# Performance work log

Measured on AMD Instinct MI355X. Metric: run time of the kernel, lower is better.

## Reference

```python
import jax, jax.numpy as jnp
import numpy as np

B, S, D, H, HD = 1, 2048, 3072, 24, 128
FFN = int(D / 3 * 8)  # 8192
ADALN = 256
NORM_EPS = 1e-6
QK_EPS = 1e-5
AXES_DIMS = (16, 56, 56)
AXES_LENS = (64, 128, 128)
THETA = 256.0


def rmsnorm(x, w, eps):
    var = jnp.mean(jnp.square(x), axis=-1, keepdims=True)
    return x * jax.lax.rsqrt(var + eps) * w


def apply_rope(x, cos, sin):
    # x: [B,S,H,HD]; cos/sin: [B,S,HD//2] (broadcast over heads, matching freqs_cis.unsqueeze(2))
    xr = x[..., 0::2]
    xi = x[..., 1::2]
    c = cos[:, :, None, :]
    s = sin[:, :, None, :]
    or_ = xr * c - xi * s
    oi_ = xr * s + xi * c
    return jnp.stack([or_, oi_], axis=-1).reshape(x.shape)


def rope_angles(ids):
    # ids: [B,S,3] int; returns angles [B,S,HD//2] concatenated per axis like RopeEmbedder
    parts = []
    for d, idx_axis in zip(AXES_DIMS, range(len(AXES_DIMS))):
        freqs = 1.0 / (THETA ** (jnp.arange(0, d, 2, dtype=jnp.float32) / d))  # [d/2]
        ang = ids[..., idx_axis].astype(jnp.float32)[..., None] * freqs  # [B,S,d/2]
        parts.append(ang)
    return jnp.concatenate(parts, axis=-1)  # [B,S,64]


def setup_inputs() -> dict:
    key = jax.random.key(0)
    ks = jax.random.split(key, 20)
    w = 0.02
    ids = jnp.concatenate([
        jax.random.randint(ks[15], (B, S, 1), 0, AXES_LENS[0]),
        jax.random.randint(ks[16], (B, S, 1), 0, AXES_LENS[1]),
        jax.random.randint(ks[17], (B, S, 1), 0, AXES_LENS[2]),
    ], axis=-1)
    return {
        "x": jax.random.normal(ks[0], (B, S, D), jnp.float32),
        "adaln_input": jax.random.normal(ks[1], (B, ADALN), jnp.float32),
        "attn_mask": jnp.ones((B, S), dtype=bool),
        "ids": ids,
        "attn_norm1_w": jnp.ones((D,), jnp.float32),
        "attn_norm2_w": jnp.ones((D,), jnp.float32),
        "ffn_norm1_w": jnp.ones((D,), jnp.float32),
        "ffn_norm2_w": jnp.ones((D,), jnp.float32),
        "norm_q_w": jnp.ones((HD,), jnp.float32),
        "norm_k_w": jnp.ones((HD,), jnp.float32),
        "wq": jax.random.normal(ks[2], (D, D), jnp.float32) * w,
        "wk": jax.random.normal(ks[3], (D, D), jnp.float32) * w,
        "wv": jax.random.normal(ks[4], (D, D), jnp.float32) * w,
        "wo": jax.random.normal(ks[5], (D, D), jnp.float32) * w,
        "w1": jax.random.normal(ks[6], (D, FFN), jnp.float32) * w,
        "w2": jax.random.normal(ks[7], (FFN, D), jnp.float32) * w,
        "w3": jax.random.normal(ks[8], (D, FFN), jnp.float32) * w,
        "adaln_w": jax.random.normal(ks[9], (ADALN, 4 * D), jnp.float32) * w,
        "adaln_b": jnp.zeros((4 * D,), jnp.float32),
    }


def block_forward(x, adaln_input, attn_mask, ids,
                  attn_norm1_w, attn_norm2_w, ffn_norm1_w, ffn_norm2_w,
                  norm_q_w, norm_k_w, wq, wk, wv, wo, w1, w2, w3,
                  adaln_w, adaln_b):
    ang = rope_angles(ids)
    cos, sin = jnp.cos(ang), jnp.sin(ang)

    mod = adaln_input @ adaln_w + adaln_b
    scale_msa, gate_msa, scale_mlp, gate_mlp = jnp.split(mod[:, None, :], 4, axis=2)
    gate_msa, gate_mlp = jnp.tanh(gate_msa), jnp.tanh(gate_mlp)
    scale_msa, scale_mlp = 1.0 + scale_msa, 1.0 + scale_mlp

    # Attention branch
    xs = rmsnorm(x, attn_norm1_w, NORM_EPS) * scale_msa  # [B,S,D]
    q = (xs @ wq).reshape(B, S, H, HD)
    k = (xs @ wk).reshape(B, S, H, HD)
    v = (xs @ wv).reshape(B, S, H, HD)
    q = rmsnorm(q, norm_q_w, QK_EPS)
    k = rmsnorm(k, norm_k_w, QK_EPS)
    q = apply_rope(q, cos, sin)
    k = apply_rope(k, cos, sin)

    scores = jnp.einsum('bqhd,bkhd->bhqk', q, k) / jnp.sqrt(jnp.float32(HD))
    neg = jnp.finfo(scores.dtype).min
    scores = jnp.where(attn_mask[:, None, None, :], scores, neg)
    probs = jax.nn.softmax(scores, axis=-1)
    attn = jnp.einsum('bhqk,bkhd->bqhd', probs, v).reshape(B, S, D)
    attn_out = attn @ wo

    x = x + gate_msa * rmsnorm(attn_out, attn_norm2_w, NORM_EPS)

    # FFN branch (SwiGLU)
    xf = rmsnorm(x, ffn_norm1_w, NORM_EPS) * scale_mlp
    h = jax.nn.silu(xf @ w1) * (xf @ w3)
    ffn_out = h @ w2
    x = x + gate_mlp * rmsnorm(ffn_out, ffn_norm2_w, NORM_EPS)
    return x


def reference(x, adaln_input, attn_mask, ids,
              attn_norm1_w, attn_norm2_w, ffn_norm1_w, ffn_norm2_w,
              norm_q_w, norm_k_w, wq, wk, wv, wo, w1, w2, w3,
              adaln_w, adaln_b):
    return block_forward(x, adaln_input, attn_mask, ids,
                         attn_norm1_w, attn_norm2_w, ffn_norm1_w, ffn_norm2_w,
                         norm_q_w, norm_k_w, wq, wk, wv, wo, w1, w2, w3,
                         adaln_w, adaln_b)
```

## Files before the change

### kernel.cpp

```cpp
#include <hip/hip_runtime.h>

#define AS1 __attribute__((address_space(1)))
#define AS3 __attribute__((address_space(3)))

typedef __bf16 bf16;
using bf16x8 = __attribute__((ext_vector_type(8))) __bf16;
using bf16x4 = __attribute__((ext_vector_type(4))) __bf16;
using bf16x2 = __attribute__((ext_vector_type(2))) __bf16;
using f32x4  = __attribute__((ext_vector_type(4))) float;


__device__ inline float wsum(float v) {
#pragma unroll
  for (int o = 32; o; o >>= 1) v += __shfl_xor(v, o, 64);
  return v;
}

template <int EPI>
__global__ __launch_bounds__(512, 1) void gemm256(
    const bf16* __restrict__ A, const bf16* __restrict__ Bt, void* __restrict__ Cv,
    int K, int lda, int ldb, int ldc, long long kOff, long long sC) {
  __shared__ bf16 lds[2][2][256 * 64];
  const int t = threadIdx.x;
  const int lane = t & 63, wid = t >> 6;
  const int wm = wid >> 2, wn = wid & 3;
  const int row16 = lane & 15, kg = lane >> 4;
  const int m0 = blockIdx.x * 256, n0 = blockIdx.y * 256;
  const int NT = K >> 6;
  const int sgran = (lane & 7) ^ (lane >> 3);
  A += (long long)blockIdx.z * kOff;
  Bt += (long long)blockIdx.z * kOff;

  auto stageA = [&](int buf, int r, int tk) {
    const int wrow = ((wid & 4) << 5) + (r << 5) + ((wid & 3) << 3);
    __builtin_amdgcn_global_load_lds(
        (const AS1 void*)(A + (long long)(m0 + wrow + (lane >> 3)) * lda + tk * 64 +
                          (sgran << 3)),
        (AS3 void*)&lds[buf][0][wrow * 64], 16, 0, 0);
  };
  auto stageB = [&](int buf, int r, int tk) {
    const int wrow = ((wid & 4) << 5) + (r << 5) + ((wid & 3) << 3);
    __builtin_amdgcn_global_load_lds(
        (const AS1 void*)(Bt + (long long)(n0 + wrow + (lane >> 3)) * ldb + tk * 64 +
                          (sgran << 3)),
        (AS3 void*)&lds[buf][1][wrow * 64], 16, 0, 0);
  };

  f32x4 acc[8][4];
#pragma unroll
  for (int i = 0; i < 8; ++i)
#pragma unroll
    for (int j = 0; j < 4; ++j) acc[i][j] = (f32x4){0.f, 0.f, 0.f, 0.f};

#pragma unroll
  for (int r = 0; r < 4; ++r) { stageA(0, r, 0); stageB(0, r, 0); }
#pragma unroll
  for (int r = 0; r < 3; ++r) { stageA(1, r, 1); stageB(1, r, 1); }

  bf16x8 bfr[4][2], af[2][2];

  for (int kt = 0; kt < NT; ++kt) {
    const int cb = kt & 1, nb = cb ^ 1;
    if (kt + 1 < NT) asm volatile("s_waitcnt vmcnt(6)" ::: "memory");
    else             asm volatile("s_waitcnt vmcnt(0)" ::: "memory");
    __builtin_amdgcn_s_barrier();

    if (kt + 1 < NT) { stageA(nb, 3, kt + 1); stageB(nb, 3, kt + 1); }
#pragma unroll
    for (int ni = 0; ni < 4; ++ni)
#pragma unroll
      for (int kk = 0; kk < 2; ++kk) {
        const int r = wn * 64 + ni * 16 + row16;
        bfr[ni][kk] = *(const bf16x8*)&lds[cb][1][r * 64 + (((kk * 4 + kg) ^ (r & 7)) << 3)];
      }
#pragma unroll
    for (int mi = 0; mi < 2; ++mi)
#pragma unroll
      for (int kk = 0; kk < 2; ++kk) {
        const int r = wm * 128 + mi * 16 + row16;
        af[mi][kk] = *(const bf16x8*)&lds[cb][0][r * 64 + (((kk * 4 + kg) ^ (r & 7)) << 3)];
      }
    __builtin_amdgcn_s_barrier();
    asm volatile("s_waitcnt lgkmcnt(0)" ::: "memory");
    __builtin_amdgcn_s_setprio(1);
#pragma unroll
    for (int kk = 0; kk < 2; ++kk)
#pragma unroll
      for (int mi = 0; mi < 2; ++mi)
#pragma unroll
        for (int ni = 0; ni < 4; ++ni)
          acc[mi][ni] =
              __builtin_amdgcn_mfma_f32_16x16x32_bf16(af[mi][kk], bfr[ni][kk], acc[mi][ni], 0, 0, 0);
    __builtin_amdgcn_s_setprio(0);

#pragma unroll
    for (int q = 1; q < 4; ++q) {
      __builtin_amdgcn_s_barrier();
      if (kt + 2 < NT) { stageA(cb, q - 1, kt + 2); stageB(cb, q - 1, kt + 2); }
#pragma unroll
      for (int mi = 0; mi < 2; ++mi)
#pragma unroll
        for (int kk = 0; kk < 2; ++kk) {
          const int r = wm * 128 + q * 32 + mi * 16 + row16;
          af[mi][kk] = *(const bf16x8*)&lds[cb][0][r * 64 + (((kk * 4 + kg) ^ (r & 7)) << 3)];
        }
      __builtin_amdgcn_s_barrier();
      asm volatile("s_waitcnt lgkmcnt(0)" ::: "memory");
      __builtin_amdgcn_s_setprio(1);
#pragma unroll
      for (int kk = 0; kk < 2; ++kk)
#pragma unroll
        for (int mi = 0; mi < 2; ++mi)
#pragma unroll
          for (int ni = 0; ni < 4; ++ni)
            acc[q * 2 + mi][ni] = __builtin_amdgcn_mfma_f32_16x16x32_bf16(
                af[mi][kk], bfr[ni][kk], acc[q * 2 + mi][ni], 0, 0, 0);
      __builtin_amdgcn_s_setprio(0);
    }
  }

  float* Cf = (float*)Cv;
  bf16* Cb = (bf16*)Cv;
  const long long cz = (long long)blockIdx.z * sC;
#pragma unroll
  for (int mf = 0; mf < 8; ++mf)
#pragma unroll
    for (int ni = 0; ni < 4; ++ni)
#pragma unroll
      for (int rr = 0; rr < 4; ++rr) {
        const int row = m0 + wm * 128 + (mf >> 1) * 32 + (mf & 1) * 16 + kg * 4 + rr;
        const int col = n0 + wn * 64 + ni * 16 + row16;
        const long long idx = cz + (long long)row * ldc + col;
        const float v = acc[mf][ni][rr];
        if constexpr (EPI == 0) Cf[idx] = v;
        else Cb[idx] = (bf16)v;
      }
}

__global__ __launch_bounds__(256) void flash_attn_k(const bf16* __restrict__ qkv,
                                                    const bf16* __restrict__ vt,
                                                    bf16* __restrict__ attn) {
  __shared__ bf16 Ks[64 * 128];
  __shared__ bf16 Vs[128 * 64];
  __shared__ bf16 Ps[4 * 32 * 64];
  const int t = threadIdx.x, lane = t & 63, wid = t >> 6;
  const int row16 = lane & 15, kg = lane >> 4;
  const int q0 = blockIdx.x * 128;
  const int h = blockIdx.y;
  const bf16* Qp = qkv + h * 128;
  const bf16* Kp = qkv + 3072 + h * 128;
  const bf16* Vt = vt + (long long)h * 262144;
  const float iscale = 0.08838834764831845f;

  bf16x8 qf[2][4];
#pragma unroll
  for (int mi = 0; mi < 2; ++mi)
#pragma unroll
    for (int kc = 0; kc < 4; ++kc)
      qf[mi][kc] = *(const bf16x8*)&Qp[(long long)(q0 + wid * 32 + mi * 16 + row16) * 9216 +
                                       kc * 32 + kg * 8];
  bf16x8 ones;
#pragma unroll
  for (int j = 0; j < 8; ++j) ones[j] = (bf16)1.0f;

  f32x4 oacc[2][8];
#pragma unroll
  for (int mi = 0; mi < 2; ++mi)
#pragma unroll
    for (int nd = 0; nd < 8; ++nd) oacc[mi][nd] = (f32x4){0.f, 0.f, 0.f, 0.f};
  f32x4 lacc[2] = {(f32x4){0.f, 0.f, 0.f, 0.f}, (f32x4){0.f, 0.f, 0.f, 0.f}};
  float mst[2][4];
#pragma unroll
  for (int mi = 0; mi < 2; ++mi)
#pragma unroll
    for (int r = 0; r < 4; ++r) mst[mi][r] = -1e30f;

  bf16* Pw = &Ps[wid * 2048];

  for (int kv0 = 0; kv0 < 2048; kv0 += 64) {
#pragma unroll
    for (int p = 0; p < 4; ++p) {
      const int gi = p * 256 + t;
      const int row = gi >> 4, g = gi & 15;
      __builtin_amdgcn_global_load_lds(
          (const AS1 void*)(Kp + (long long)(kv0 + row) * 9216 + ((g ^ (row & 7)) << 3)),
          (AS3 void*)&Ks[(p * 256 + wid * 64) * 8], 16, 0, 0);
    }
#pragma unroll
    for (int p = 0; p < 4; ++p) {
      const int gi = p * 256 + t;
      const int row = gi >> 3, g = gi & 7;
      __builtin_amdgcn_global_load_lds(
          (const AS1 void*)(Vt + (long long)row * 2048 + kv0 + ((g ^ (row & 7)) << 3)),
          (AS3 void*)&Vs[(p * 256 + wid * 64) * 8], 16, 0, 0);
    }
    __syncthreads();

    f32x4 sacc[2][4];
#pragma unroll
    for (int mi = 0; mi < 2; ++mi)
#pragma unroll
      for (int nf = 0; nf < 4; ++nf) sacc[mi][nf] = (f32x4){0.f, 0.f, 0.f, 0.f};
#pragma unroll
    for (int kc = 0; kc < 4; ++kc) {
      bf16x8 kf[4];
#pragma unroll
      for (int nf = 0; nf < 4; ++nf) {
        const int row = nf * 16 + row16;
        kf[nf] = *(const bf16x8*)&Ks[(row * 16 + ((kc * 4 + kg) ^ (row & 7))) * 8];
      }
#pragma unroll
      for (int mi = 0; mi < 2; ++mi)
#pragma unroll
        for (int nf = 0; nf < 4; ++nf)
          sacc[mi][nf] =
              __builtin_amdgcn_mfma_f32_16x16x32_bf16(qf[mi][kc], kf[nf], sacc[mi][nf], 0, 0, 0);
    }

    float fac[2][4];
#pragma unroll
    for (int mi = 0; mi < 2; ++mi)
#pragma unroll
      for (int r = 0; r < 4; ++r) {
        float rm = sacc[mi][0][r];
#pragma unroll
        for (int nf = 1; nf < 4; ++nf) rm = fmaxf(rm, sacc[mi][nf][r]);
        rm = fmaxf(rm, __shfl_xor(rm, 1, 64));
        rm = fmaxf(rm, __shfl_xor(rm, 2, 64));
        rm = fmaxf(rm, __shfl_xor(rm, 4, 64));
        rm = fmaxf(rm, __shfl_xor(rm, 8, 64));
        const float mnew = fmaxf(mst[mi][r], rm * iscale);
        fac[mi][r] = __expf(mst[mi][r] - mnew);
        mst[mi][r] = mnew;
#pragma unroll
        for (int nf = 0; nf < 4; ++nf)
          sacc[mi][nf][r] = __expf(sacc[mi][nf][r] * iscale - mnew);
      }
#pragma unroll
    for (int mi = 0; mi < 2; ++mi)
#pragma unroll
      for (int r = 0; r < 4; ++r) {
        lacc[mi][r] *= fac[mi][r];
#pragma unroll
        for (int nd = 0; nd < 8; ++nd) oacc[mi][nd][r] *= fac[mi][r];
      }

#pragma unroll
    for (int mi = 0; mi < 2; ++mi)
#pragma unroll
      for (int nf = 0; nf < 4; ++nf)
#pragma unroll
        for (int r = 0; r < 4; ++r) {
          const int row = mi * 16 + kg * 4 + r;
          const int col = nf * 16 + row16;
          Pw[(row * 8 + ((col >> 3) ^ (row & 7))) * 8 + (col & 7)] = (bf16)sacc[mi][nf][r];
        }

#pragma unroll
    for (int kvc = 0; kvc < 2; ++kvc) {
      bf16x8 pf[2], vf[8];
#pragma unroll
      for (int mi = 0; mi < 2; ++mi) {
        const int row = mi * 16 + row16;
        pf[mi] = *(const bf16x8*)&Pw[(row * 8 + ((kvc * 4 + kg) ^ (row & 7))) * 8];
      }
#pragma unroll
      for (int nd = 0; nd < 8; ++nd) {
        const int row = nd * 16 + row16;
        vf[nd] = *(const bf16x8*)&Vs[(row * 8 + ((kvc * 4 + kg) ^ (row & 7))) * 8];
      }
#pragma unroll
      for (int mi = 0; mi < 2; ++mi) {
        lacc[mi] = __builtin_amdgcn_mfma_f32_16x16x32_bf16(pf[mi], ones, lacc[mi], 0, 0, 0);
#pragma unroll
        for (int nd = 0; nd < 8; ++nd)
          oacc[mi][nd] =
              __builtin_amdgcn_mfma_f32_16x16x32_bf16(pf[mi], vf[nd], oacc[mi][nd], 0, 0, 0);
      }
    }
    __syncthreads();
  }

#pragma unroll
  for (int mi = 0; mi < 2; ++mi) {
    float inv[4];
#pragma unroll
    for (int r = 0; r < 4; ++r) inv[r] = 1.f / lacc[mi][r];
#pragma unroll
    for (int nd = 0; nd < 8; ++nd)
#pragma unroll
      for (int r = 0; r < 4; ++r) {
        const int row = q0 + wid * 32 + mi * 16 + kg * 4 + r;
        const int col = h * 128 + nd * 16 + row16;
        attn[(long long)row * 3072 + col] = (bf16)(oacc[mi][nd][r] * inv[r]);
      }
  }
}

__device__ inline void convT_tile(const float* __restrict__ in, bf16* __restrict__ out,
                                  int R, int C, int bx, int by) {
  __shared__ float tile[64][65];
  const int t = threadIdx.x;
  const int r0 = by * 64, c0 = bx * 64;
#pragma unroll
  for (int it = 0; it < 4; ++it) {
    const int idx = it * 256 + t;
    const int rl = idx >> 4, c4 = (idx & 15) << 2;
    const float4 v = *(const float4*)&in[(long long)(r0 + rl) * C + c0 + c4];
    tile[rl][c4 + 0] = v.x;
    tile[rl][c4 + 1] = v.y;
    tile[rl][c4 + 2] = v.z;
    tile[rl][c4 + 3] = v.w;
  }
  __syncthreads();
#pragma unroll
  for (int it = 0; it < 4; ++it) {
    const int idx = it * 256 + t;
    const int cl = idx >> 4, r4 = (idx & 15) << 2;
    bf16x4 o;
    o[0] = (bf16)tile[r4 + 0][cl];
    o[1] = (bf16)tile[r4 + 1][cl];
    o[2] = (bf16)tile[r4 + 2][cl];
    o[3] = (bf16)tile[r4 + 3][cl];
    *(bf16x4*)&out[(long long)(c0 + cl) * R + r0 + r4] = o;
  }
}

__global__ __launch_bounds__(256) void convAll(
    const float* __restrict__ wq, const float* __restrict__ wk,
    const float* __restrict__ wv, const float* __restrict__ wo,
    const float* __restrict__ w1, const float* __restrict__ w3,
    const float* __restrict__ w2, bf16* __restrict__ wqkvT, bf16* __restrict__ woT,
    bf16* __restrict__ w13T, bf16* __restrict__ w2T) {
  const int id = blockIdx.x;
  if (id < 9216) {
    const int m = id / 2304, l = id % 2304;
    const float* in = m == 0 ? wq : m == 1 ? wk : m == 2 ? wv : wo;
    bf16* out = m < 3 ? wqkvT + (long long)m * 9437184 : woT;
    convT_tile(in, out, 3072, 3072, l % 48, l / 48);
  } else if (id < 21504) {
    int l = id - 9216;
    const int m = l / 6144;
    l %= 6144;
    convT_tile(m ? w3 : w1, w13T + (long long)m * 25165824, 3072, 8192, l % 128, l / 128);
  } else {
    const int l = id - 21504;
    convT_tile(w2, w2T, 8192, 3072, l % 48, l / 48);
  }
}

__global__ __launch_bounds__(256) void ropetab_k(const int* __restrict__ ids,
                                                 float* __restrict__ cosT,
                                                 float* __restrict__ sinT) {
  const int i = blockIdx.x * 256 + threadIdx.x;
  const int s = i >> 6, j = i & 63;
  int ax, fi;
  float d;
  if (j < 8) { ax = 0; fi = j; d = 16.f; }
  else if (j < 36) { ax = 1; fi = j - 8; d = 56.f; }
  else { ax = 2; fi = j - 36; d = 56.f; }
  const float freq = exp2f(-16.f * (float)fi / d);
  const float ang = (float)ids[s * 3 + ax] * freq;
  cosT[i] = cosf(ang);
  sinT[i] = sinf(ang);
}

__global__ __launch_bounds__(256) void adaln_kernel(const float* __restrict__ ain,
                                                    const float* __restrict__ W,
                                                    const float* __restrict__ b,
                                                    float* __restrict__ out) {
  __shared__ float a[256];
  const int t = threadIdx.x;
  a[t] = ain[t];
  __syncthreads();
  const int n = blockIdx.x * 256 + t;
  float acc = b[n];
  for (int k = 0; k < 256; ++k) acc = fmaf(a[k], W[(long long)k * 12288 + n], acc);
  const int chunk = n / 3072;
  out[n] = (chunk & 1) ? tanhf(acc) : (1.f + acc);
}

__global__ __launch_bounds__(256) void rmsnorm_scale_k(const float* __restrict__ x,
                                                       const float* __restrict__ w,
                                                       const float* __restrict__ scale,
                                                       bf16* __restrict__ out) {
  __shared__ float red[4];
  const int t = threadIdx.x, lane = t & 63, wid = t >> 6;
  const long long base = (long long)blockIdx.x * 3072;
  float v[12];
  float ss = 0.f;
#pragma unroll
  for (int ch = 0; ch < 3; ++ch) {
    const float4 f = *(const float4*)&x[base + ch * 1024 + t * 4];
    v[ch * 4 + 0] = f.x; v[ch * 4 + 1] = f.y; v[ch * 4 + 2] = f.z; v[ch * 4 + 3] = f.w;
    ss += f.x * f.x + f.y * f.y + f.z * f.z + f.w * f.w;
  }
  ss = wsum(ss);
  if (!lane) red[wid] = ss;
  __syncthreads();
  const float r = rsqrtf((red[0] + red[1] + red[2] + red[3]) / 3072.f + 1e-6f);
#pragma unroll
  for (int ch = 0; ch < 3; ++ch) {
    const int col = ch * 1024 + t * 4;
    bf16x4 o;
#pragma unroll
    for (int j = 0; j < 4; ++j) o[j] = (bf16)(v[ch * 4 + j] * r * w[col + j] * scale[col + j]);
    *(bf16x4*)&out[base + col] = o;
  }
}

__global__ __launch_bounds__(256) void qknorm_rope_k(bf16* __restrict__ qkv,
                                                     const float* __restrict__ cosT,
                                                     const float* __restrict__ sinT,
                                                     const float* __restrict__ wq,
                                                     const float* __restrict__ wk) {
  const int t = threadIdx.x, lane = t & 63, wid = t >> 6;
  const int idx = blockIdx.x * 4 + wid;
  const int s = idx / 24, h = idx % 24;
  const int isK = blockIdx.y;
  bf16* base = qkv + (long long)s * 9216 + isK * 3072 + h * 128;
  bf16x2 p = *(const bf16x2*)(base + 2 * lane);
  float xr = (float)p[0], xi = (float)p[1];
  const float ss = wsum(xr * xr + xi * xi);
  const float r = rsqrtf(ss / 128.f + 1e-5f);
  const float* w = isK ? wk : wq;
  const float2 wv = *(const float2*)&w[2 * lane];
  xr *= r * wv.x;
  xi *= r * wv.y;
  const float c = cosT[s * 64 + lane], sn = sinT[s * 64 + lane];
  bf16x2 o;
  o[0] = (bf16)(xr * c - xi * sn);
  o[1] = (bf16)(xr * sn + xi * c);
  *(bf16x2*)(base + 2 * lane) = o;
}

__global__ __launch_bounds__(256) void vtrans_k(const bf16* __restrict__ qkv,
                                                bf16* __restrict__ vt) {
  __shared__ bf16 tile[64][72];
  const int t = threadIdx.x;
  const int s0 = blockIdx.x * 64, d0 = blockIdx.y * 64, h = blockIdx.z;
#pragma unroll
  for (int it = 0; it < 2; ++it) {
    const int idx = it * 256 + t;
    const int sl = idx >> 3, c8 = (idx & 7) << 3;
    const bf16x8 v =
        *(const bf16x8*)&qkv[(long long)(s0 + sl) * 9216 + 6144 + h * 128 + d0 + c8];
    *(bf16x8*)&tile[sl][c8] = v;
  }
  __syncthreads();
#pragma unroll
  for (int it = 0; it < 2; ++it) {
    const int idx = it * 256 + t;
    const int dl = idx >> 3, s8 = (idx & 7) << 3;
    bf16x8 o;
#pragma unroll
    for (int j = 0; j < 8; ++j) o[j] = tile[s8 + j][dl];
    *(bf16x8*)&vt[(long long)h * 262144 + (long long)(d0 + dl) * 2048 + s0 + s8] = o;
  }
}

__global__ __launch_bounds__(256) void silumul_k(const bf16* __restrict__ t13,
                                                 bf16* __restrict__ h) {
  const int gi = blockIdx.x * 256 + threadIdx.x;
  const int s = gi >> 10, j8 = (gi & 1023) << 3;
  const bf16x8 a = *(const bf16x8*)&t13[(long long)s * 16384 + j8];
  const bf16x8 b = *(const bf16x8*)&t13[(long long)s * 16384 + 8192 + j8];
  bf16x8 o;
#pragma unroll
  for (int j = 0; j < 8; ++j) {
    const float x = (float)a[j];
    const float sl = x / (1.f + __expf(-x));
    o[j] = (bf16)(sl * (float)b[j]);
  }
  *(bf16x8*)&h[(long long)s * 8192 + j8] = o;
}

__global__ __launch_bounds__(256) void resid1_k(
    const float* __restrict__ x, const float* __restrict__ p0, const float* __restrict__ p1,
    const float* __restrict__ n2w, const float* __restrict__ gate,
    const float* __restrict__ f1w, const float* __restrict__ smlp,
    float* __restrict__ x1, bf16* __restrict__ xf) {
  __shared__ float red[8];
  const int t = threadIdx.x, lane = t & 63, wid = t >> 6;
  const long long base = (long long)blockIdx.x * 3072;
  float av[12];
  float ss = 0.f;
#pragma unroll
  for (int ch = 0; ch < 3; ++ch) {
    const float4 f0 = *(const float4*)&p0[base + ch * 1024 + t * 4];
    const float4 f1 = *(const float4*)&p1[base + ch * 1024 + t * 4];
    const float a0 = f0.x + f1.x, a1 = f0.y + f1.y, a2 = f0.z + f1.z, a3 = f0.w + f1.w;
    av[ch * 4 + 0] = a0; av[ch * 4 + 1] = a1; av[ch * 4 + 2] = a2; av[ch * 4 + 3] = a3;
    ss += a0 * a0 + a1 * a1 + a2 * a2 + a3 * a3;
  }
  ss = wsum(ss);
  if (!lane) red[wid] = ss;
  __syncthreads();
  const float r = rsqrtf((red[0] + red[1] + red[2] + red[3]) / 3072.f + 1e-6f);
  float xv[12];
  float ss2 = 0.f;
#pragma unroll
  for (int ch = 0; ch < 3; ++ch) {
    const int col = ch * 1024 + t * 4;
    const float4 f = *(const float4*)&x[base + col];
    float4 o;
    o.x = f.x + gate[col + 0] * (av[ch * 4 + 0] * r * n2w[col + 0]);
    o.y = f.y + gate[col + 1] * (av[ch * 4 + 1] * r * n2w[col + 1]);
    o.z = f.z + gate[col + 2] * (av[ch * 4 + 2] * r * n2w[col + 2]);
    o.w = f.w + gate[col + 3] * (av[ch * 4 + 3] * r * n2w[col + 3]);
    *(float4*)&x1[base + col] = o;
    xv[ch * 4 + 0] = o.x; xv[ch * 4 + 1] = o.y; xv[ch * 4 + 2] = o.z; xv[ch * 4 + 3] = o.w;
    ss2 += o.x * o.x + o.y * o.y + o.z * o.z + o.w * o.w;
  }
  ss2 = wsum(ss2);
  if (!lane) red[4 + wid] = ss2;
  __syncthreads();
  const float r2 = rsqrtf((red[4] + red[5] + red[6] + red[7]) / 3072.f + 1e-6f);
#pragma unroll
  for (int ch = 0; ch < 3; ++ch) {
    const int col = ch * 1024 + t * 4;
    bf16x4 o;
#pragma unroll
    for (int j = 0; j < 4; ++j)
      o[j] = (bf16)(xv[ch * 4 + j] * r2 * f1w[col + j] * smlp[col + j]);
    *(bf16x4*)&xf[base + col] = o;
  }
}

__global__ __launch_bounds__(256) void resid2_k(const float* __restrict__ x1,
                                                const float* __restrict__ f0,
                                                const float* __restrict__ f1,
                                                const float* __restrict__ nw,
                                                const float* __restrict__ gate,
                                                float* __restrict__ out) {
  __shared__ float red[4];
  const int t = threadIdx.x, lane = t & 63, wid = t >> 6;
  const long long base = (long long)blockIdx.x * 3072;
  float fv[12];
  float ss = 0.f;
#pragma unroll
  for (int ch = 0; ch < 3; ++ch) {
    const float4 a = *(const float4*)&f0[base + ch * 1024 + t * 4];
    const float4 b = *(const float4*)&f1[base + ch * 1024 + t * 4];
    const float a0 = a.x + b.x, a1 = a.y + b.y, a2 = a.z + b.z, a3 = a.w + b.w;
    fv[ch * 4 + 0] = a0; fv[ch * 4 + 1] = a1; fv[ch * 4 + 2] = a2; fv[ch * 4 + 3] = a3;
    ss += a0 * a0 + a1 * a1 + a2 * a2 + a3 * a3;
  }
  ss = wsum(ss);
  if (!lane) red[wid] = ss;
  __syncthreads();
  const float r = rsqrtf((red[0] + red[1] + red[2] + red[3]) / 3072.f + 1e-6f);
#pragma unroll
  for (int ch = 0; ch < 3; ++ch) {
    const int col = ch * 1024 + t * 4;
    const float4 f = *(const float4*)&x1[base + col];
    float4 o;
    o.x = f.x + gate[col + 0] * (fv[ch * 4 + 0] * r * nw[col + 0]);
    o.y = f.y + gate[col + 1] * (fv[ch * 4 + 1] * r * nw[col + 1]);
    o.z = f.z + gate[col + 2] * (fv[ch * 4 + 2] * r * nw[col + 2]);
    o.w = f.w + gate[col + 3] * (fv[ch * 4 + 3] * r * nw[col + 3]);
    *(float4*)&out[base + col] = o;
  }
}

extern "C" void kernel_launch(void* const* d_in, const int* in_sizes, int n_in,
                              void* d_out, int out_size, void* d_ws, size_t ws_size,
                              hipStream_t stream) {
  const float* x    = (const float*)d_in[0];
  const float* ain  = (const float*)d_in[1];
  const int* ids    = (const int*)d_in[3];
  const float* n1w  = (const float*)d_in[4];
  const float* n2w  = (const float*)d_in[5];
  const float* fn1w = (const float*)d_in[6];
  const float* fn2w = (const float*)d_in[7];
  const float* nqw  = (const float*)d_in[8];
  const float* nkw  = (const float*)d_in[9];
  const float* wq   = (const float*)d_in[10];
  const float* wk   = (const float*)d_in[11];
  const float* wv   = (const float*)d_in[12];
  const float* wo   = (const float*)d_in[13];
  const float* w1   = (const float*)d_in[14];
  const float* w2   = (const float*)d_in[15];
  const float* w3   = (const float*)d_in[16];
  const float* adw  = (const float*)d_in[17];
  const float* adb  = (const float*)d_in[18];

  if (ws_size < 395362304ULL) return;

  char* ws = (char*)d_ws;
  bf16* wqkvT = (bf16*)(ws + 0LL);
  bf16* woT   = (bf16*)(ws + 56623104LL);
  bf16* w13T  = (bf16*)(ws + 75497472LL);
  bf16* w2T   = (bf16*)(ws + 176160768LL);
  float* cosT = (float*)(ws + 226492416LL);
  float* sinT = (float*)(ws + 227016704LL);
  float* adv  = (float*)(ws + 227540992LL);
  bf16* xs    = (bf16*)(ws + 227590144LL);
  char* big   = ws + 240173056LL;
  float* x1   = (float*)(big);
  bf16* qkv   = (bf16*)(big + 25165824LL);
  bf16* vt    = (bf16*)(big + 62914560LL);
  bf16* attn  = (bf16*)(big + 75497472LL);
  float* aoP  = (float*)(big + 88080384LL);
  bf16* t13   = (bf16*)(big + 25165824LL);
  bf16* hbuf  = (bf16*)(big + 92274688LL);
  float* ffnP = (float*)(big + 25165824LL);

  const dim3 b256(256);
  const dim3 b512(512);

  ropetab_k<<<dim3(512), b256, 0, stream>>>(ids, cosT, sinT);
  adaln_kernel<<<dim3(48), b256, 0, stream>>>(ain, adw, adb, adv);

  convAll<<<dim3(27648), b256, 0, stream>>>(wq, wk, wv, wo, w1, w3, w2, wqkvT, woT, w13T,
                                            w2T);

  rmsnorm_scale_k<<<dim3(2048), b256, 0, stream>>>(x, n1w, adv, xs);

  gemm256<1><<<dim3(8, 36, 1), b512, 0, stream>>>(xs, wqkvT, qkv, 3072, 3072, 3072, 9216,
                                                  0LL, 0LL);

  qknorm_rope_k<<<dim3(12288, 2), b256, 0, stream>>>(qkv, cosT, sinT, nqw, nkw);
  vtrans_k<<<dim3(32, 2, 24), b256, 0, stream>>>(qkv, vt);

  flash_attn_k<<<dim3(16, 24), b256, 0, stream>>>(qkv, vt, attn);

  gemm256<0><<<dim3(8, 12, 2), b512, 0, stream>>>(attn, woT, aoP, 1536, 3072, 3072, 3072,
                                                  1536LL, 6291456LL);
  resid1_k<<<dim3(2048), b256, 0, stream>>>(x, aoP, aoP + 6291456LL, n2w, adv + 3072, fn1w,
                                            adv + 6144, x1, xs);
  gemm256<1><<<dim3(8, 64, 1), b512, 0, stream>>>(xs, w13T, t13, 3072, 3072, 3072, 16384,
                                                  0LL, 0LL);
  silumul_k<<<dim3(8192), b256, 0, stream>>>(t13, hbuf);
  gemm256<0><<<dim3(8, 12, 2), b512, 0, stream>>>(hbuf, w2T, ffnP, 4096, 8192, 8192, 3072,
                                                  4096LL, 6291456LL);
  resid2_k<<<dim3(2048), b256, 0, stream>>>(x1, ffnP, ffnP + 6291456LL, fn2w, adv + 9216,
                                            (float*)d_out);
}
```

Baseline: 911.3 us.

## Use 32x32 MFMA in GEMM and split-KV flash attention with combine kernel

The GEMM inner loop moves from 16x16x32 to 32x32x16 bf16 MFMA tiles, which cuts the number of LDS fragment reads per MFMA and changes the accumulator layout and epilogue indexing. Flash attention now splits the KV range into two halves across blockIdx.z, doubling the grid from 384 blocks so more of the GPU's compute units are busy. Each half writes unnormalized fp32 partial outputs plus per-row max and sum, and a new combine kernel merges them into bf16. The split adds extra fp32 traffic to and from memory and one more kernel launch.

```diff
diff --git a/kernel.cpp b/kernel.cpp
--- a/kernel.cpp
+++ b/kernel.cpp
@@ -8,6 +8,7 @@
 using bf16x4 = __attribute__((ext_vector_type(4))) __bf16;
 using bf16x2 = __attribute__((ext_vector_type(2))) __bf16;
 using f32x4  = __attribute__((ext_vector_type(4))) float;
+using f32x16 = __attribute__((ext_vector_type(16))) float;
 
 
 __device__ inline float wsum(float v) {
@@ -24,7 +25,7 @@
   const int t = threadIdx.x;
   const int lane = t & 63, wid = t >> 6;
   const int wm = wid >> 2, wn = wid & 3;
-  const int row16 = lane & 15, kg = lane >> 4;
+  const int l31 = lane & 31, hi = lane >> 5;
   const int m0 = blockIdx.x * 256, n0 = blockIdx.y * 256;
   const int NT = K >> 6;
   const int sgran = (lane & 7) ^ (lane >> 3);
@@ -46,18 +47,20 @@
         (AS3 void*)&lds[buf][1][wrow * 64], 16, 0, 0);
   };
 
-  f32x4 acc[8][4];
-#pragma unroll
-  for (int i = 0; i < 8; ++i)
-#pragma unroll
-    for (int j = 0; j < 4; ++j) acc[i][j] = (f32x4){0.f, 0.f, 0.f, 0.f};
+  f32x16 acc[4][2];
+#pragma unroll
+  for (int i = 0; i < 4; ++i)
+#pragma unroll
+    for (int j = 0; j < 2; ++j)
+#pragma unroll
+      for (int e = 0; e < 16; ++e) acc[i][j][e] = 0.f;
 
 #pragma unroll
   for (int r = 0; r < 4; ++r) { stageA(0, r, 0); stageB(0, r, 0); }
 #pragma unroll
   for (int r = 0; r < 3; ++r) { stageA(1, r, 1); stageB(1, r, 1); }
 
-  bf16x8 bfr[4][2], af[2][2];
+  bf16x8 bfr[2][4], af[4];
 
   for (int kt = 0; kt < NT; ++kt) {
     const int cb = kt & 1, nb = cb ^ 1;
@@ -67,54 +70,49 @@
 
     if (kt + 1 < NT) { stageA(nb, 3, kt + 1); stageB(nb, 3, kt + 1); }
 #pragma unroll
-    for (int ni = 0; ni < 4; ++ni)
-#pragma unroll
-      for (int kk = 0; kk < 2; ++kk) {
-        const int r = wn * 64 + ni * 16 + row16;
-        bfr[ni][kk] = *(const bf16x8*)&lds[cb][1][r * 64 + (((kk * 4 + kg) ^ (r & 7)) << 3)];
-      }
-#pragma unroll
-    for (int mi = 0; mi < 2; ++mi)
-#pragma unroll
-      for (int kk = 0; kk < 2; ++kk) {
-        const int r = wm * 128 + mi * 16 + row16;
-        af[mi][kk] = *(const bf16x8*)&lds[cb][0][r * 64 + (((kk * 4 + kg) ^ (r & 7)) << 3)];
-      }
+    for (int ni = 0; ni < 2; ++ni)
+#pragma unroll
+      for (int ks = 0; ks < 4; ++ks) {
+        const int r = wn * 64 + ni * 32 + l31;
+        bfr[ni][ks] =
+            *(const bf16x8*)&lds[cb][1][r * 64 + (((ks * 2 + hi) ^ (r & 7)) << 3)];
+      }
+    {
+      const int r = wm * 128 + l31;
+#pragma unroll
+      for (int ks = 0; ks < 4; ++ks)
+        af[ks] = *(const bf16x8*)&lds[cb][0][r * 64 + (((ks * 2 + hi) ^ (r & 7)) << 3)];
+    }
     __builtin_amdgcn_s_barrier();
     asm volatile("s_waitcnt lgkmcnt(0)" ::: "memory");
     __builtin_amdgcn_s_setprio(1);
 #pragma unroll
-    for (int kk = 0; kk < 2; ++kk)
-#pragma unroll
-      for (int mi = 0; mi < 2; ++mi)
-#pragma unroll
-        for (int ni = 0; ni < 4; ++ni)
-          acc[mi][ni] =
-              __builtin_amdgcn_mfma_f32_16x16x32_bf16(af[mi][kk], bfr[ni][kk], acc[mi][ni], 0, 0, 0);
+    for (int ks = 0; ks < 4; ++ks)
+#pragma unroll
+      for (int ni = 0; ni < 2; ++ni)
+        acc[0][ni] =
+            __builtin_amdgcn_mfma_f32_32x32x16_bf16(af[ks], bfr[ni][ks], acc[0][ni], 0, 0, 0);
     __builtin_amdgcn_s_setprio(0);
 
 #pragma unroll
     for (int q = 1; q < 4; ++q) {
       __builtin_amdgcn_s_barrier();
       if (kt + 2 < NT) { stageA(cb, q - 1, kt + 2); stageB(cb, q - 1, kt + 2); }
-#pragma unroll
-      for (int mi = 0; mi < 2; ++mi)
-#pragma unroll
-        for (int kk = 0; kk < 2; ++kk) {
-          const int r = wm * 128 + q * 32 + mi * 16 + row16;
-          af[mi][kk] = *(const bf16x8*)&lds[cb][0][r * 64 + (((kk * 4 + kg) ^ (r & 7)) << 3)];
-        }
+      {
+        const int r = wm * 128 + q * 32 + l31;
+#pragma unroll
+        for (int ks = 0; ks < 4; ++ks)
+          af[ks] = *(const bf16x8*)&lds[cb][0][r * 64 + (((ks * 2 + hi) ^ (r & 7)) << 3)];
+      }
       __builtin_amdgcn_s_barrier();
       asm volatile("s_waitcnt lgkmcnt(0)" ::: "memory");
       __builtin_amdgcn_s_setprio(1);
 #pragma unroll
-      for (int kk = 0; kk < 2; ++kk)
-#pragma unroll
-        for (int mi = 0; mi < 2; ++mi)
-#pragma unroll
-          for (int ni = 0; ni < 4; ++ni)
-            acc[q * 2 + mi][ni] = __builtin_amdgcn_mfma_f32_16x16x32_bf16(
-                af[mi][kk], bfr[ni][kk], acc[q * 2 + mi][ni], 0, 0, 0);
+      for (int ks = 0; ks < 4; ++ks)
+#pragma unroll
+        for (int ni = 0; ni < 2; ++ni)
+          acc[q][ni] = __builtin_amdgcn_mfma_f32_32x32x16_bf16(af[ks], bfr[ni][ks],
+                                                              acc[q][ni], 0, 0, 0);
       __builtin_amdgcn_s_setprio(0);
     }
   }
@@ -123,15 +121,15 @@
   bf16* Cb = (bf16*)Cv;
   const long long cz = (long long)blockIdx.z * sC;
 #pragma unroll
-  for (int mf = 0; mf < 8; ++mf)
-#pragma unroll
-    for (int ni = 0; ni < 4; ++ni)
-#pragma unroll
-      for (int rr = 0; rr < 4; ++rr) {
-        const int row = m0 + wm * 128 + (mf >> 1) * 32 + (mf & 1) * 16 + kg * 4 + rr;
-        const int col = n0 + wn * 64 + ni * 16 + row16;
+  for (int mi = 0; mi < 4; ++mi)
+#pragma unroll
+    for (int ni = 0; ni < 2; ++ni)
+#pragma unroll
+      for (int reg = 0; reg < 16; ++reg) {
+        const int row = m0 + wm * 128 + mi * 32 + (reg & 3) + ((reg >> 2) << 3) + (hi << 2);
+        const int col = n0 + wn * 64 + ni * 32 + l31;
         const long long idx = cz + (long long)row * ldc + col;
-        const float v = acc[mf][ni][rr];
+        const float v = acc[mi][ni][reg];
         if constexpr (EPI == 0) Cf[idx] = v;
         else Cb[idx] = (bf16)v;
       }
@@ -139,7 +137,8 @@
 
 __global__ __launch_bounds__(256) void flash_attn_k(const bf16* __restrict__ qkv,
                                                     const bf16* __restrict__ vt,
-                                                    bf16* __restrict__ attn) {
+                                                    float* __restrict__ Op,
+                                                    float* __restrict__ mlp) {
   __shared__ bf16 Ks[64 * 128];
   __shared__ bf16 Vs[128 * 64];
   __shared__ bf16 Ps[4 * 32 * 64];
@@ -147,6 +146,7 @@
   const int row16 = lane & 15, kg = lane >> 4;
   const int q0 = blockIdx.x * 128;
   const int h = blockIdx.y;
+  const int z = blockIdx.z;
   const bf16* Qp = qkv + h * 128;
   const bf16* Kp = qkv + 3072 + h * 128;
   const bf16* Vt = vt + (long long)h * 262144;
@@ -176,8 +176,9 @@
     for (int r = 0; r < 4; ++r) mst[mi][r] = -1e30f;
 
   bf16* Pw = &Ps[wid * 2048];
-
-  for (int kv0 = 0; kv0 < 2048; kv0 += 64) {
+  const int kvbase = z << 10;
+
+  for (int kv0 = kvbase; kv0 < kvbase + 1024; kv0 += 64) {
 #pragma unroll
     for (int p = 0; p < 4; ++p) {
       const int gi = p * 256 + t;
@@ -281,20 +282,48 @@
     __syncthreads();
   }
 
-#pragma unroll
-  for (int mi = 0; mi < 2; ++mi) {
-    float inv[4];
-#pragma unroll
-    for (int r = 0; r < 4; ++r) inv[r] = 1.f / lacc[mi][r];
+  float* Oz = Op + (long long)z * 6291456;
+#pragma unroll
+  for (int mi = 0; mi < 2; ++mi)
 #pragma unroll
     for (int nd = 0; nd < 8; ++nd)
 #pragma unroll
       for (int r = 0; r < 4; ++r) {
         const int row = q0 + wid * 32 + mi * 16 + kg * 4 + r;
         const int col = h * 128 + nd * 16 + row16;
-        attn[(long long)row * 3072 + col] = (bf16)(oacc[mi][nd][r] * inv[r]);
-      }
-  }
+        Oz[(long long)row * 3072 + col] = oacc[mi][nd][r];
+      }
+  if (row16 == 0) {
+#pragma unroll
+    for (int mi = 0; mi < 2; ++mi)
+#pragma unroll
+      for (int r = 0; r < 4; ++r) {
+        const int s = q0 + wid * 32 + mi * 16 + kg * 4 + r;
+        const long long mi2 = ((long long)z * 49152 + s * 24 + h) * 2;
+        mlp[mi2] = mst[mi][r];
+        mlp[mi2 + 1] = lacc[mi][r];
+      }
+  }
+}
+
+__global__ __launch_bounds__(256) void fa_combine_k(const float* __restrict__ Op,
+                                                    const float* __restrict__ mlp,
+                                                    bf16* __restrict__ attn) {
+  const int t = threadIdx.x, lane = t & 63, wid = t >> 6;
+  const int pair = blockIdx.x * 4 + wid;
+  const int s = pair / 24, h = pair % 24;
+  const float2 ml0 = *(const float2*)&mlp[(long long)pair * 2];
+  const float2 ml1 = *(const float2*)&mlp[(49152LL + pair) * 2];
+  const float m = fmaxf(ml0.x, ml1.x);
+  const float a0 = __expf(ml0.x - m), a1 = __expf(ml1.x - m);
+  const float inv = 1.f / (ml0.y * a0 + ml1.y * a1);
+  const long long base = (long long)s * 3072 + h * 128 + lane * 2;
+  const float2 o0 = *(const float2*)&Op[base];
+  const float2 o1 = *(const float2*)&Op[6291456LL + base];
+  bf16x2 o;
+  o[0] = (bf16)((o0.x * a0 + o1.x * a1) * inv);
+  o[1] = (bf16)((o0.y * a0 + o1.y * a1) * inv);
+  *(bf16x2*)&attn[base] = o;
 }
 
 __device__ inline void convT_tile(const float* __restrict__ in, bf16* __restrict__ out,
@@ -602,6 +631,8 @@
   bf16* vt    = (bf16*)(big + 62914560LL);
   bf16* attn  = (bf16*)(big + 75497472LL);
   float* aoP  = (float*)(big + 88080384LL);
+  float* Opart= (float*)(big + 88080384LL);
+  float* mlp  = (float*)(big + 138412032LL);
   bf16* t13   = (bf16*)(big + 25165824LL);
   bf16* hbuf  = (bf16*)(big + 92274688LL);
   float* ffnP = (float*)(big + 25165824LL);
@@ -623,7 +654,8 @@
   qknorm_rope_k<<<dim3(12288, 2), b256, 0, stream>>>(qkv, cosT, sinT, nqw, nkw);
   vtrans_k<<<dim3(32, 2, 24), b256, 0, stream>>>(qkv, vt);
 
-  flash_attn_k<<<dim3(16, 24), b256, 0, stream>>>(qkv, vt, attn);
+  flash_attn_k<<<dim3(16, 24, 2), b256, 0, stream>>>(qkv, vt, Opart, mlp);
+  fa_combine_k<<<dim3(12288), b256, 0, stream>>>(Opart, mlp, attn);
 
   gemm256<0><<<dim3(8, 12, 2), b512, 0, stream>>>(attn, woT, aoP, 1536, 3072, 3072, 3072,
                                                   1536LL, 6291456LL);
```

Measured after the change: 930.6 us. +2.1%, slower.

## Split flash attention over two KV halves and merge with combine kernel

Applied to the files above, without the earlier changes.

The attention kernel now launches with a z dimension of 2, so each block processes half of the KV sequence. It writes unnormalized fp32 partial outputs plus per-row max and sum to workspace. A new combine kernel rescales and merges the two partials into the bf16 attention output. This doubles the grid from 384 to 768 blocks to fill the 256 CUs better, at the cost of extra fp32 partial traffic and one more kernel launch.

```diff
diff --git a/kernel.cpp b/kernel.cpp
--- a/kernel.cpp
+++ b/kernel.cpp
@@ -139,7 +139,8 @@
 
 __global__ __launch_bounds__(256) void flash_attn_k(const bf16* __restrict__ qkv,
                                                     const bf16* __restrict__ vt,
-                                                    bf16* __restrict__ attn) {
+                                                    float* __restrict__ Op,
+                                                    float* __restrict__ mlp) {
   __shared__ bf16 Ks[64 * 128];
   __shared__ bf16 Vs[128 * 64];
   __shared__ bf16 Ps[4 * 32 * 64];
@@ -147,6 +148,7 @@
   const int row16 = lane & 15, kg = lane >> 4;
   const int q0 = blockIdx.x * 128;
   const int h = blockIdx.y;
+  const int z = blockIdx.z;
   const bf16* Qp = qkv + h * 128;
   const bf16* Kp = qkv + 3072 + h * 128;
   const bf16* Vt = vt + (long long)h * 262144;
@@ -176,8 +178,9 @@
     for (int r = 0; r < 4; ++r) mst[mi][r] = -1e30f;
 
   bf16* Pw = &Ps[wid * 2048];
-
-  for (int kv0 = 0; kv0 < 2048; kv0 += 64) {
+  const int kvbase = z << 10;
+
+  for (int kv0 = kvbase; kv0 < kvbase + 1024; kv0 += 64) {
 #pragma unroll
     for (int p = 0; p < 4; ++p) {
       const int gi = p * 256 + t;
@@ -281,20 +284,48 @@
     __syncthreads();
   }
 
-#pragma unroll
-  for (int mi = 0; mi < 2; ++mi) {
-    float inv[4];
-#pragma unroll
-    for (int r = 0; r < 4; ++r) inv[r] = 1.f / lacc[mi][r];
+  float* Oz = Op + (long long)z * 6291456;
+#pragma unroll
+  for (int mi = 0; mi < 2; ++mi)
 #pragma unroll
     for (int nd = 0; nd < 8; ++nd)
 #pragma unroll
       for (int r = 0; r < 4; ++r) {
         const int row = q0 + wid * 32 + mi * 16 + kg * 4 + r;
         const int col = h * 128 + nd * 16 + row16;
-        attn[(long long)row * 3072 + col] = (bf16)(oacc[mi][nd][r] * inv[r]);
-      }
-  }
+        Oz[(long long)row * 3072 + col] = oacc[mi][nd][r];
+      }
+  if (row16 == 0) {
+#pragma unroll
+    for (int mi = 0; mi < 2; ++mi)
+#pragma unroll
+      for (int r = 0; r < 4; ++r) {
+        const int s = q0 + wid * 32 + mi * 16 + kg * 4 + r;
+        const long long mi2 = ((long long)z * 49152 + s * 24 + h) * 2;
+        mlp[mi2] = mst[mi][r];
+        mlp[mi2 + 1] = lacc[mi][r];
+      }
+  }
+}
+
+__global__ __launch_bounds__(256) void fa_combine_k(const float* __restrict__ Op,
+                                                    const float* __restrict__ mlp,
+                                                    bf16* __restrict__ attn) {
+  const int t = threadIdx.x, lane = t & 63, wid = t >> 6;
+  const int pair = blockIdx.x * 4 + wid;
+  const int s = pair / 24, h = pair % 24;
+  const float2 ml0 = *(const float2*)&mlp[(long long)pair * 2];
+  const float2 ml1 = *(const float2*)&mlp[(49152LL + pair) * 2];
+  const float m = fmaxf(ml0.x, ml1.x);
+  const float a0 = __expf(ml0.x - m), a1 = __expf(ml1.x - m);
+  const float inv = 1.f / (ml0.y * a0 + ml1.y * a1);
+  const long long base = (long long)s * 3072 + h * 128 + lane * 2;
+  const float2 o0 = *(const float2*)&Op[base];
+  const float2 o1 = *(const float2*)&Op[6291456LL + base];
+  bf16x2 o;
+  o[0] = (bf16)((o0.x * a0 + o1.x * a1) * inv);
+  o[1] = (bf16)((o0.y * a0 + o1.y * a1) * inv);
+  *(bf16x2*)&attn[base] = o;
 }
 
 __device__ inline void convT_tile(const float* __restrict__ in, bf16* __restrict__ out,
@@ -602,6 +633,8 @@
   bf16* vt    = (bf16*)(big + 62914560LL);
   bf16* attn  = (bf16*)(big + 75497472LL);
   float* aoP  = (float*)(big + 88080384LL);
+  float* Opart= (float*)(big + 88080384LL);
+  float* mlp  = (float*)(big + 138412032LL);
   bf16* t13   = (bf16*)(big + 25165824LL);
   bf16* hbuf  = (bf16*)(big + 92274688LL);
   float* ffnP = (float*)(big + 25165824LL);
@@ -623,7 +656,8 @@
   qknorm_rope_k<<<dim3(12288, 2), b256, 0, stream>>>(qkv, cosT, sinT, nqw, nkw);
   vtrans_k<<<dim3(32, 2, 24), b256, 0, stream>>>(qkv, vt);
 
-  flash_attn_k<<<dim3(16, 24), b256, 0, stream>>>(qkv, vt, attn);
+  flash_attn_k<<<dim3(16, 24, 2), b256, 0, stream>>>(qkv, vt, Opart, mlp);
+  fa_combine_k<<<dim3(12288), b256, 0, stream>>>(Opart, mlp, attn);
 
   gemm256<0><<<dim3(8, 12, 2), b512, 0, stream>>>(attn, woT, aoP, 1536, 3072, 3072, 3072,
                                                   1536LL, 6291456LL);
```

After: 886.1 us. 1.03x faster.
